# Performance work log

Measured on AMD Instinct MI355X. Metric: run time of the kernel, lower is better.

## Reference

```python
import jax, jax.numpy as jnp
import numpy as np

N_NODES = 100000
K_STEPS = 10
ALPHA = 0.1


def setup_inputs() -> dict:
    key = jax.random.key(0)
    k1, k2, k3, k4 = jax.random.split(key, 4)
    x = jax.random.normal(k1, (N_NODES, 512), dtype=jnp.float32)
    edge_index = jax.random.randint(k2, (2, 3200000), 0, N_NODES, dtype=jnp.int64)
    W1 = jax.random.normal(k3, (512, 256), dtype=jnp.float32) * (1.0 / np.sqrt(512))
    b1 = jnp.zeros((256,), dtype=jnp.float32)
    W2 = jax.random.normal(k4, (256, 64), dtype=jnp.float32) * (1.0 / np.sqrt(256))
    b2 = jnp.zeros((64,), dtype=jnp.float32)
    return {"x": x, "edge_index": edge_index, "W1": W1, "b1": b1, "W2": W2, "b2": b2}


def _gcn_norm(edge_index, num_nodes):
    # Add self loops and compute symmetric normalization deg^-1/2 A deg^-1/2.
    loops = jnp.arange(num_nodes, dtype=edge_index.dtype)
    src = jnp.concatenate([edge_index[0], loops])
    dst = jnp.concatenate([edge_index[1], loops])
    deg = jax.ops.segment_sum(jnp.ones_like(dst, dtype=jnp.float32), dst,
                              num_segments=num_nodes)
    dinv = jnp.where(deg > 0, jax.lax.rsqrt(deg), 0.0)
    norm = dinv[src] * dinv[dst]  # [E + N]
    return src, dst, norm


def reference(x, edge_index, W1, b1, W2, b2):
    n = x.shape[0]
    # MLP (dropout is identity at inference)
    h = jax.nn.relu(x @ W1 + b1)
    h = h @ W2 + b2  # [N, C]
    # APPNP propagation: h_{k+1} = (1-alpha) * A_hat h_k + alpha * h_0
    src, dst, norm = _gcn_norm(edge_index, n)
    h0 = h

    def step(carry, _):
        msg = carry[src] * norm[:, None]                     # gather + scale
        agg = jax.ops.segment_sum(msg, dst, num_segments=n)  # scatter-add
        return (1.0 - ALPHA) * agg + ALPHA * h0, None

    h, _ = jax.lax.scan(step, h, None, length=K_STEPS)
    return jax.nn.log_softmax(h, axis=1)
```

## Files before the change

kernel.cpp:

```cpp
#include <hip/hip_runtime.h>
#include <cstdint>
#include <cstddef>


typedef _Float16 half8 __attribute__((ext_vector_type(8)));
typedef float floatx4 __attribute__((ext_vector_type(4)));

__device__ inline float2 unpack2(uint u) {
    union { uint u; _Float16 h[2]; } c; c.u = u;
    return make_float2((float)c.h[0], (float)c.h[1]);
}
__device__ inline uint pack2(float a, float b) {
    union { uint u; _Float16 h[2]; } c; c.h[0] = (_Float16)a; c.h[1] = (_Float16)b;
    return c.u;
}

__global__ void transpose_w1c(const float* __restrict__ W1, _Float16* __restrict__ W1tc) {
    int i = blockIdx.x * 256 + threadIdx.x;
    if (i < 512 * 256) {
        int kt = i >> 13, ctile = (i >> 9) & 15, col = (i >> 5) & 15, j = i & 31;
        W1tc[i] = (_Float16)W1[(size_t)(kt * 32 + j) * 256 + ctile * 16 + col];
    }
}
__global__ void transpose_w2c(const float* __restrict__ W2, _Float16* __restrict__ W2tc) {
    int i = blockIdx.x * 256 + threadIdx.x;
    if (i < 256 * 64) {
        int kt = i >> 11, ct = (i >> 9) & 3, col = (i >> 5) & 15, j = i & 31;
        W2tc[i] = (_Float16)W2[(size_t)(kt * 32 + j) * 64 + ct * 16 + col];
    }
}

__global__ __launch_bounds__(256) void mlp_kernel(
    const float* __restrict__ x, const _Float16* __restrict__ W1tc,
    const float* __restrict__ b1, const _Float16* __restrict__ W2tc,
    const float* __restrict__ b2, const float* __restrict__ dinv,
    _Float16* __restrict__ g0h, int n)
{
    __shared__ __align__(16) _Float16 xs[32][520];
    __shared__ __align__(16) _Float16 hmid[32][264];

    const int tid  = threadIdx.x;
    const int lane = tid & 63;
    const int wid  = tid >> 6;
    const int r0blk = blockIdx.x * 32;
    const int lr = lane & 15;
    const int lg = lane >> 4;

    for (int fi = tid; fi < 32 * 128; fi += 256) {
        int r = fi >> 7, k4 = (fi & 127) * 4;
        float4 v = *(const float4*)(x + (size_t)(r0blk + r) * 512 + k4);
        union { short4 s; _Float16 h[4]; } c;
        c.h[0] = (_Float16)v.x; c.h[1] = (_Float16)v.y;
        c.h[2] = (_Float16)v.z; c.h[3] = (_Float16)v.w;
        *(short4*)&xs[r][k4] = c.s;
    }
    __syncthreads();

    floatx4 acc1[2][4];
#pragma unroll
    for (int c = 0; c < 4; ++c) {
        float b = b1[wid * 64 + c * 16 + lr];
        acc1[0][c] = (floatx4){b, b, b, b};
        acc1[1][c] = (floatx4){b, b, b, b};
    }

#pragma unroll 2
    for (int kt = 0; kt < 16; ++kt) {
        half8 bf[4];
#pragma unroll
        for (int c = 0; c < 4; ++c)
            bf[c] = *(const half8*)&W1tc[(((size_t)kt * 16 + wid * 4 + c) * 16 + lr) * 32 + lg * 8];
        half8 a0 = *(const half8*)&xs[lr][kt * 32 + lg * 8];
        half8 a1 = *(const half8*)&xs[16 + lr][kt * 32 + lg * 8];
#pragma unroll
        for (int c = 0; c < 4; ++c) {
            acc1[0][c] = __builtin_amdgcn_mfma_f32_16x16x32_f16(a0, bf[c], acc1[0][c], 0, 0, 0);
            acc1[1][c] = __builtin_amdgcn_mfma_f32_16x16x32_f16(a1, bf[c], acc1[1][c], 0, 0, 0);
        }
    }

#pragma unroll
    for (int rt = 0; rt < 2; ++rt)
#pragma unroll
        for (int c = 0; c < 4; ++c)
#pragma unroll
            for (int r = 0; r < 4; ++r) {
                float v = fmaxf(acc1[rt][c][r], 0.f);
                hmid[rt * 16 + lg * 4 + r][wid * 64 + c * 16 + lr] = (_Float16)v;
            }
    __syncthreads();

    const int rt = wid >> 1, ct2 = (wid & 1) * 2;
    floatx4 acc2[2] = {(floatx4){0,0,0,0}, (floatx4){0,0,0,0}};
#pragma unroll
    for (int kt = 0; kt < 8; ++kt) {
        half8 a = *(const half8*)&hmid[rt * 16 + lr][kt * 32 + lg * 8];
#pragma unroll
        for (int q = 0; q < 2; ++q) {
            half8 b = *(const half8*)&W2tc[((size_t)(kt * 4 + ct2 + q) * 16 + lr) * 32 + lg * 8];
            acc2[q] = __builtin_amdgcn_mfma_f32_16x16x32_f16(a, b, acc2[q], 0, 0, 0);
        }
    }
#pragma unroll
    for (int q = 0; q < 2; ++q) {
        int col = (ct2 + q) * 16 + lr;
        float bb = b2[col];
#pragma unroll
        for (int r = 0; r < 4; ++r) {
            int row = r0blk + rt * 16 + lg * 4 + r;
            float di = dinv[row];
            g0h[(size_t)row * 64 + col] = (_Float16)(di * (acc2[q][r] + bb));
        }
    }
}

__global__ void init_counts_kernel(int* __restrict__ counts, int n) {
    int i = blockIdx.x * blockDim.x + threadIdx.x;
    if (i < n) counts[i] = 1;
}

__global__ void count_kernel(const int* __restrict__ dstL, int* __restrict__ counts,
                             int e, int rs, int n) {
    const int r = blockIdx.x & 7;
    const int g = blockIdx.x >> 3;
    const int B = gridDim.x >> 3;
    const int lo = r * rs;
    const int hi = min(lo + rs, n);
    for (int i = g * blockDim.x + threadIdx.x; i < e; i += B * blockDim.x) {
        int d = dstL[i];
        if (d >= lo && d < hi) atomicAdd(&counts[d], 1);
    }
}

__global__ void dinv_kernel(const int* __restrict__ counts, float* __restrict__ dinv,
                            float* __restrict__ Anode, int n) {
    int i = blockIdx.x * blockDim.x + threadIdx.x;
    if (i < n) {
        float deg = (float)counts[i];
        dinv[i] = 1.0f / sqrtf(deg);
        Anode[i] = 0.9f / deg;
    }
}

__global__ __launch_bounds__(256) void scan_a(const int* __restrict__ counts,
                                              int* __restrict__ rowptr,
                                              int* __restrict__ bsums, int n)
{
    __shared__ int s[256];
    const int t = threadIdx.x;
    const int i = blockIdx.x * 256 + t;
    int v = (i < n) ? (counts[i] - 1) : 0;
    s[t] = v;
    __syncthreads();
    for (int off = 1; off < 256; off <<= 1) {
        int add = (t >= off) ? s[t - off] : 0;
        __syncthreads();
        s[t] += add;
        __syncthreads();
    }
    if (i < n) rowptr[i] = s[t] - v;
    if (t == 255) bsums[blockIdx.x] = s[255];
}

__global__ __launch_bounds__(512) void scan_b(const int* __restrict__ bsums,
                                              int* __restrict__ boff, int nb)
{
    __shared__ int s[512];
    const int t = threadIdx.x;
    int v = (t < nb) ? bsums[t] : 0;
    s[t] = v;
    __syncthreads();
    for (int off = 1; off < 512; off <<= 1) {
        int add = (t >= off) ? s[t - off] : 0;
        __syncthreads();
        s[t] += add;
        __syncthreads();
    }
    if (t < nb) boff[t] = s[t] - v;
}

__global__ __launch_bounds__(256) void scan_c(int* __restrict__ rowptr,
                                              int* __restrict__ cursor,
                                              const int* __restrict__ boff, int n, int e)
{
    int i = blockIdx.x * 256 + threadIdx.x;
    if (i < n) {
        int v = rowptr[i] + boff[blockIdx.x];
        rowptr[i] = v;
        cursor[i] = v;
    }
    if (i == 0) rowptr[n] = e;
}

__global__ void fill_kernel(const int* __restrict__ srcL, const int* __restrict__ dstL,
                            int* __restrict__ cursor, int* __restrict__ srcs,
                            int e, int rs, int n) {
    const int r = blockIdx.x & 7;
    const int g = blockIdx.x >> 3;
    const int B = gridDim.x >> 3;
    const int lo = r * rs;
    const int hi = min(lo + rs, n);
    for (int i = g * blockDim.x + threadIdx.x; i < e; i += B * blockDim.x) {
        int d = dstL[i];
        if (d >= lo && d < hi) {
            int pos = atomicAdd(&cursor[d], 1);
            srcs[pos] = srcL[i];
        }
    }
}

__global__ __launch_bounds__(256) void prop_kernel(
    const uint* __restrict__ gu, const uint* __restrict__ g0u,
    uint* __restrict__ gnu, const int* __restrict__ rowptr,
    const int* __restrict__ srcs, const float* __restrict__ Anode, int n)
{
    const int node = (blockIdx.x * blockDim.x + threadIdx.x) >> 6;
    if (node >= n) return;
    const int lane = threadIdx.x & 63;
    const int half_ = lane >> 5;
    const int p = lane & 31;
    const int e0 = rowptr[node], e1 = rowptr[node + 1];
    float accx = 0.f, accy = 0.f;
    int e = e0 + half_;
    for (; e + 14 < e1; e += 16) {
        int s0 = srcs[e],      s1 = srcs[e + 2],  s2 = srcs[e + 4],  s3 = srcs[e + 6];
        int s4 = srcs[e + 8],  s5 = srcs[e + 10], s6 = srcs[e + 12], s7 = srcs[e + 14];
        float2 f0 = unpack2(gu[(size_t)s0 * 32 + p]);
        float2 f1 = unpack2(gu[(size_t)s1 * 32 + p]);
        float2 f2 = unpack2(gu[(size_t)s2 * 32 + p]);
        float2 f3 = unpack2(gu[(size_t)s3 * 32 + p]);
        float2 f4 = unpack2(gu[(size_t)s4 * 32 + p]);
        float2 f5 = unpack2(gu[(size_t)s5 * 32 + p]);
        float2 f6 = unpack2(gu[(size_t)s6 * 32 + p]);
        float2 f7 = unpack2(gu[(size_t)s7 * 32 + p]);
        accx += f0.x; accy += f0.y;
        accx += f1.x; accy += f1.y;
        accx += f2.x; accy += f2.y;
        accx += f3.x; accy += f3.y;
        accx += f4.x; accy += f4.y;
        accx += f5.x; accy += f5.y;
        accx += f6.x; accy += f6.y;
        accx += f7.x; accy += f7.y;
    }
    for (; e < e1; e += 2) {
        float2 f = unpack2(gu[(size_t)srcs[e] * 32 + p]);
        accx += f.x; accy += f.y;
    }
    accx += __shfl_xor(accx, 32);
    accy += __shfl_xor(accy, 32);

    const float A = Anode[node];
    float2 self = unpack2(gu[(size_t)node * 32 + p]);
    float2 anc  = unpack2(g0u[(size_t)node * 32 + p]);
    float ox = A * (accx + self.x) + 0.1f * anc.x;
    float oy = A * (accy + self.y) + 0.1f * anc.y;
    if (half_ == 0) gnu[(size_t)node * 32 + p] = pack2(ox, oy);
}

__global__ __launch_bounds__(256) void logsoftmax_kernel(
    const _Float16* __restrict__ g, const float* __restrict__ dinv,
    float* __restrict__ out, int n)
{
    const int row = (blockIdx.x * blockDim.x + threadIdx.x) >> 6;
    const int lane = threadIdx.x & 63;
    if (row >= n) return;
    float v = (float)g[(size_t)row * 64 + lane] / dinv[row];
    float m = v;
#pragma unroll
    for (int o = 32; o > 0; o >>= 1) m = fmaxf(m, __shfl_xor(m, o));
    float ex = expf(v - m);
    float s = ex;
#pragma unroll
    for (int o = 32; o > 0; o >>= 1) s += __shfl_xor(s, o);
    out[(size_t)row * 64 + lane] = v - m - logf(s);
}

extern "C" void kernel_launch(void* const* d_in, const int* in_sizes, int n_in,
                              void* d_out, int out_size, void* d_ws, size_t ws_size,
                              hipStream_t stream)
{
    const float* x  = (const float*)d_in[0];
    const int*   ei = (const int*)d_in[1];
    const float* W1 = (const float*)d_in[2];
    const float* b1 = (const float*)d_in[3];
    const float* W2 = (const float*)d_in[4];
    const float* b2 = (const float*)d_in[5];
    float* out = (float*)d_out;

    const int n = in_sizes[0] / 512;
    const int e = in_sizes[1] / 2;
    const int* srcL = ei;
    const int* dstL = ei + e;

    char* wsb = (char*)d_ws;
    size_t off = 0;
    auto alloc = [&](size_t bytes) -> void* {
        void* p = wsb + off;
        off = (off + bytes + 255) & ~(size_t)255;
        return p;
    };
    _Float16* g0h = (_Float16*)alloc((size_t)n * 64 * 2);
    _Float16* gp0 = (_Float16*)alloc((size_t)n * 64 * 2);
    _Float16* gp1 = (_Float16*)alloc((size_t)n * 64 * 2);
    int*   srcs   = (int*)alloc((size_t)e * 4);
    float* dinv   = (float*)alloc((size_t)n * 4);
    float* Anode  = (float*)alloc((size_t)n * 4);
    int*   counts = (int*)alloc((size_t)n * 4);
    int*   rowptr = (int*)alloc((size_t)(n + 1) * 4);
    int*   bsums  = (int*)alloc(4096);
    int*   boff   = (int*)alloc(4096);
    _Float16* W1tc = (_Float16*)alloc((size_t)512 * 256 * 2);
    _Float16* W2tc = (_Float16*)alloc((size_t)256 * 64 * 2);
    int* cursor = counts;

    const int nb = (n + 255) / 256;
    const int rs = (n + 7) / 8;

    transpose_w1c<<<(512 * 256 + 255) / 256, 256, 0, stream>>>(W1, W1tc);
    transpose_w2c<<<(256 * 64 + 255) / 256, 256, 0, stream>>>(W2, W2tc);

    init_counts_kernel<<<nb, 256, 0, stream>>>(counts, n);
    count_kernel<<<1024, 256, 0, stream>>>(dstL, counts, e, rs, n);
    dinv_kernel<<<nb, 256, 0, stream>>>(counts, dinv, Anode, n);
    scan_a<<<nb, 256, 0, stream>>>(counts, rowptr, bsums, n);
    scan_b<<<1, 512, 0, stream>>>(bsums, boff, nb);
    scan_c<<<nb, 256, 0, stream>>>(rowptr, cursor, boff, n, e);
    fill_kernel<<<1024, 256, 0, stream>>>(srcL, dstL, cursor, srcs, e, rs, n);

    mlp_kernel<<<n / 32, 256, 0, stream>>>(x, W1tc, b1, W2tc, b2, dinv, g0h, n);

    const int pgrid = (n * 64 + 255) / 256;
    const uint* gin = (const uint*)g0h;
    uint* bufs[2] = {(uint*)gp0, (uint*)gp1};
    for (int it = 0; it < 10; ++it) {
        uint* gn = bufs[it & 1];
        prop_kernel<<<pgrid, 256, 0, stream>>>(gin, (const uint*)g0h, gn,
                                               rowptr, srcs, Anode, n);
        gin = gn;
    }
    logsoftmax_kernel<<<pgrid, 256, 0, stream>>>((const _Float16*)gin, dinv, out, n);
}
```

Before: 1.435 ms.

## Split propagation gathers into four source-range buckets for cache locality

Edges are sorted within each destination by which quarter of the source range they fall in, and each propagation step runs four passes, one per bucket. Each pass then gathers from only a quarter of the feature table, so that slice can stay resident in cache. In exchange there are four times as many launches, partial sums are written to and read back from global memory in fp16 between passes, and the preprocessing needs extra count and cursor arrays.

```diff
diff --git a/kernel.cpp b/kernel.cpp
--- a/kernel.cpp
+++ b/kernel.cpp
@@ -114,13 +114,15 @@
     }
 }
 
-__global__ void init_counts_kernel(int* __restrict__ counts, int n) {
+__global__ void init_counts_kernel(int* __restrict__ counts, int* __restrict__ count2, int n) {
     int i = blockIdx.x * blockDim.x + threadIdx.x;
+    if (i < 4 * n) count2[i] = 0;
     if (i < n) counts[i] = 1;
 }
 
-__global__ void count_kernel(const int* __restrict__ dstL, int* __restrict__ counts,
-                             int e, int rs, int n) {
+__global__ void count_kernel(const int* __restrict__ srcL, const int* __restrict__ dstL,
+                             int* __restrict__ counts, int* __restrict__ count2,
+                             int e, int rs, int n, int bsize) {
     const int r = blockIdx.x & 7;
     const int g = blockIdx.x >> 3;
     const int B = gridDim.x >> 3;
@@ -128,7 +130,11 @@
     const int hi = min(lo + rs, n);
     for (int i = g * blockDim.x + threadIdx.x; i < e; i += B * blockDim.x) {
         int d = dstL[i];
-        if (d >= lo && d < hi) atomicAdd(&counts[d], 1);
+        if (d >= lo && d < hi) {
+            atomicAdd(&counts[d], 1);
+            int b = srcL[i] / bsize;
+            atomicAdd(&count2[d * 4 + b], 1);
+        }
     }
 }
 
@@ -180,21 +186,31 @@
 }
 
 __global__ __launch_bounds__(256) void scan_c(int* __restrict__ rowptr,
-                                              int* __restrict__ cursor,
-                                              const int* __restrict__ boff, int n, int e)
+                                              const int* __restrict__ boff, int n)
 {
     int i = blockIdx.x * 256 + threadIdx.x;
+    if (i < n) rowptr[i] += boff[blockIdx.x];
+}
+
+__global__ void bptr_init(const int* __restrict__ rowptr, const int* __restrict__ count2,
+                          int* __restrict__ bptr, int* __restrict__ cursor2, int n, int e)
+{
+    int i = blockIdx.x * blockDim.x + threadIdx.x;
     if (i < n) {
-        int v = rowptr[i] + boff[blockIdx.x];
-        rowptr[i] = v;
-        cursor[i] = v;
-    }
-    if (i == 0) rowptr[n] = e;
+        int base = rowptr[i];
+#pragma unroll
+        for (int b = 0; b < 4; ++b) {
+            bptr[i * 4 + b] = base;
+            cursor2[i * 4 + b] = base;
+            base += count2[i * 4 + b];
+        }
+    }
+    if (i == 0) bptr[4 * n] = e;
 }
 
 __global__ void fill_kernel(const int* __restrict__ srcL, const int* __restrict__ dstL,
-                            int* __restrict__ cursor, int* __restrict__ srcs,
-                            int e, int rs, int n) {
+                            int* __restrict__ cursor2, int* __restrict__ srcs,
+                            int e, int rs, int n, int bsize) {
     const int r = blockIdx.x & 7;
     const int g = blockIdx.x >> 3;
     const int B = gridDim.x >> 3;
@@ -203,58 +219,63 @@
     for (int i = g * blockDim.x + threadIdx.x; i < e; i += B * blockDim.x) {
         int d = dstL[i];
         if (d >= lo && d < hi) {
-            int pos = atomicAdd(&cursor[d], 1);
-            srcs[pos] = srcL[i];
-        }
-    }
-}
-
-__global__ __launch_bounds__(256) void prop_kernel(
+            int s = srcL[i];
+            int b = s / bsize;
+            int pos = atomicAdd(&cursor2[d * 4 + b], 1);
+            srcs[pos] = s;
+        }
+    }
+}
+
+__global__ __launch_bounds__(256) void prop_pass(
     const uint* __restrict__ gu, const uint* __restrict__ g0u,
-    uint* __restrict__ gnu, const int* __restrict__ rowptr,
-    const int* __restrict__ srcs, const float* __restrict__ Anode, int n)
+    uint* __restrict__ accb, const int* __restrict__ bptr,
+    const int* __restrict__ srcs, const float* __restrict__ Anode,
+    int n, int mode, int bucket)
 {
     const int node = (blockIdx.x * blockDim.x + threadIdx.x) >> 6;
     if (node >= n) return;
     const int lane = threadIdx.x & 63;
     const int half_ = lane >> 5;
     const int p = lane & 31;
-    const int e0 = rowptr[node], e1 = rowptr[node + 1];
-    float accx = 0.f, accy = 0.f;
-    int e = e0 + half_;
-    for (; e + 14 < e1; e += 16) {
-        int s0 = srcs[e],      s1 = srcs[e + 2],  s2 = srcs[e + 4],  s3 = srcs[e + 6];
-        int s4 = srcs[e + 8],  s5 = srcs[e + 10], s6 = srcs[e + 12], s7 = srcs[e + 14];
-        float2 f0 = unpack2(gu[(size_t)s0 * 32 + p]);
-        float2 f1 = unpack2(gu[(size_t)s1 * 32 + p]);
-        float2 f2 = unpack2(gu[(size_t)s2 * 32 + p]);
-        float2 f3 = unpack2(gu[(size_t)s3 * 32 + p]);
-        float2 f4 = unpack2(gu[(size_t)s4 * 32 + p]);
-        float2 f5 = unpack2(gu[(size_t)s5 * 32 + p]);
-        float2 f6 = unpack2(gu[(size_t)s6 * 32 + p]);
-        float2 f7 = unpack2(gu[(size_t)s7 * 32 + p]);
-        accx += f0.x; accy += f0.y;
-        accx += f1.x; accy += f1.y;
-        accx += f2.x; accy += f2.y;
-        accx += f3.x; accy += f3.y;
-        accx += f4.x; accy += f4.y;
-        accx += f5.x; accy += f5.y;
-        accx += f6.x; accy += f6.y;
-        accx += f7.x; accy += f7.y;
-    }
-    for (; e < e1; e += 2) {
-        float2 f = unpack2(gu[(size_t)srcs[e] * 32 + p]);
-        accx += f.x; accy += f.y;
-    }
-    accx += __shfl_xor(accx, 32);
-    accy += __shfl_xor(accy, 32);
-
-    const float A = Anode[node];
-    float2 self = unpack2(gu[(size_t)node * 32 + p]);
-    float2 anc  = unpack2(g0u[(size_t)node * 32 + p]);
-    float ox = A * (accx + self.x) + 0.1f * anc.x;
-    float oy = A * (accy + self.y) + 0.1f * anc.y;
-    if (half_ == 0) gnu[(size_t)node * 32 + p] = pack2(ox, oy);
+    int e = bptr[node * 4 + bucket] + half_;
+    const int e1 = bptr[node * 4 + bucket + 1];
+    float ax = 0.f, ay = 0.f;
+    while (e < e1) {
+        const int e1m1 = e1 - 1;
+        int idx[8], ss[8];
+#pragma unroll
+        for (int k = 0; k < 8; ++k) {
+            idx[k] = e + 2 * k;
+            ss[k] = srcs[min(idx[k], e1m1)];
+        }
+        float2 f[8];
+#pragma unroll
+        for (int k = 0; k < 8; ++k)
+            f[k] = unpack2(gu[(size_t)ss[k] * 32 + p]);
+#pragma unroll
+        for (int k = 0; k < 8; ++k)
+            if (idx[k] < e1) { ax += f[k].x; ay += f[k].y; }
+        e += 16;
+    }
+    ax += __shfl_xor(ax, 32);
+    ay += __shfl_xor(ay, 32);
+    if (half_ == 1) return;
+    const size_t ro = (size_t)node * 32 + p;
+    if (mode == 0) {
+        accb[ro] = pack2(ax, ay);
+    } else if (mode == 1) {
+        float2 a0 = unpack2(accb[ro]);
+        accb[ro] = pack2(a0.x + ax, a0.y + ay);
+    } else {
+        float2 a0 = unpack2(accb[ro]);
+        const float A = Anode[node];
+        float2 self = unpack2(gu[ro]);
+        float2 anc  = unpack2(g0u[ro]);
+        float ox = A * (a0.x + ax + self.x) + 0.1f * anc.x;
+        float oy = A * (a0.y + ay + self.y) + 0.1f * anc.y;
+        accb[ro] = pack2(ox, oy);
+    }
 }
 
 __global__ __launch_bounds__(256) void logsoftmax_kernel(
@@ -306,26 +327,30 @@
     float* dinv   = (float*)alloc((size_t)n * 4);
     float* Anode  = (float*)alloc((size_t)n * 4);
     int*   counts = (int*)alloc((size_t)n * 4);
+    int*   count2 = (int*)alloc((size_t)n * 16);
     int*   rowptr = (int*)alloc((size_t)(n + 1) * 4);
+    int*   bptr   = (int*)alloc((size_t)(4 * n + 1) * 4);
+    int*   cursor2= (int*)alloc((size_t)n * 16);
     int*   bsums  = (int*)alloc(4096);
     int*   boff   = (int*)alloc(4096);
     _Float16* W1tc = (_Float16*)alloc((size_t)512 * 256 * 2);
     _Float16* W2tc = (_Float16*)alloc((size_t)256 * 64 * 2);
-    int* cursor = counts;
-
-    const int nb = (n + 255) / 256;
-    const int rs = (n + 7) / 8;
+
+    const int nb  = (n + 255) / 256;
+    const int rs  = (n + 7) / 8;
+    const int bsize = (n + 3) / 4;
 
     transpose_w1c<<<(512 * 256 + 255) / 256, 256, 0, stream>>>(W1, W1tc);
     transpose_w2c<<<(256 * 64 + 255) / 256, 256, 0, stream>>>(W2, W2tc);
 
-    init_counts_kernel<<<nb, 256, 0, stream>>>(counts, n);
-    count_kernel<<<1024, 256, 0, stream>>>(dstL, counts, e, rs, n);
+    init_counts_kernel<<<(4 * n + 255) / 256, 256, 0, stream>>>(counts, count2, n);
+    count_kernel<<<1024, 256, 0, stream>>>(srcL, dstL, counts, count2, e, rs, n, bsize);
     dinv_kernel<<<nb, 256, 0, stream>>>(counts, dinv, Anode, n);
     scan_a<<<nb, 256, 0, stream>>>(counts, rowptr, bsums, n);
     scan_b<<<1, 512, 0, stream>>>(bsums, boff, nb);
-    scan_c<<<nb, 256, 0, stream>>>(rowptr, cursor, boff, n, e);
-    fill_kernel<<<1024, 256, 0, stream>>>(srcL, dstL, cursor, srcs, e, rs, n);
+    scan_c<<<nb, 256, 0, stream>>>(rowptr, boff, n);
+    bptr_init<<<nb, 256, 0, stream>>>(rowptr, count2, bptr, cursor2, n, e);
+    fill_kernel<<<1024, 256, 0, stream>>>(srcL, dstL, cursor2, srcs, e, rs, n, bsize);
 
     mlp_kernel<<<n / 32, 256, 0, stream>>>(x, W1tc, b1, W2tc, b2, dinv, g0h, n);
 
@@ -333,10 +358,13 @@
     const uint* gin = (const uint*)g0h;
     uint* bufs[2] = {(uint*)gp0, (uint*)gp1};
     for (int it = 0; it < 10; ++it) {
-        uint* gn = bufs[it & 1];
-        prop_kernel<<<pgrid, 256, 0, stream>>>(gin, (const uint*)g0h, gn,
-                                               rowptr, srcs, Anode, n);
-        gin = gn;
+        uint* acc = bufs[it & 1];
+        for (int b = 0; b < 4; ++b) {
+            int mode = (b == 0) ? 0 : ((b == 3) ? 2 : 1);
+            prop_pass<<<pgrid, 256, 0, stream>>>(gin, (const uint*)g0h, acc,
+                                                 bptr, srcs, Anode, n, mode, b);
+        }
+        gin = acc;
     }
     logsoftmax_kernel<<<pgrid, 256, 0, stream>>>((const _Float16*)gin, dinv, out, n);
 }
```

After: 1.979 ms. 37.9% more time.
